# Performance work log

Hardware: AMD Instinct MI355X
Metric: run time of the kernel (lower is better)

Reference implementation:

```python
import jax, jax.numpy as jnp
import numpy as np

BN_EPS = 1e-5
DIST_MIN = 1e-10


def _three_nn(p1t, p2t):
    # p1t: [B,N,3], p2t: [B,S,3] -> squared dists/idx of 3 nearest, [B,N,3]
    d2 = (jnp.sum(p1t * p1t, -1, keepdims=True)
          - 2.0 * jnp.einsum('bnc,bsc->bns', p1t, p2t)
          + jnp.sum(p2t * p2t, -1)[:, None, :])  # [B,N,S]
    neg, idx = jax.lax.top_k(-d2, 3)
    return -neg, idx


def _gather_knn(f2t, idx):
    # f2t: [B,S,D], idx: [B,N,3] -> [B,N,3,D]
    return jax.vmap(lambda f, i: f[i])(f2t, idx)


def _conv_bn_relu(x, W, b, g, beta):
    # x: [B,C,N]; 1x1 conv == channel GEMM, then train-mode BN, then ReLU
    y = jnp.einsum('oc,bcn->bon', W, x) + b[None, :, None]
    mean = jnp.mean(y, axis=(0, 2), keepdims=True)
    var = jnp.mean((y - mean) ** 2, axis=(0, 2), keepdims=True)
    yn = (y - mean) * jax.lax.rsqrt(var + BN_EPS)
    return jax.nn.relu(yn * g[None, :, None] + beta[None, :, None])


def setup_inputs() -> dict:
    key = jax.random.key(0)
    ks = jax.random.split(key, 10)
    B, N, S, D1, D2 = 4, 8192, 2048, 128, 256
    C_in, C_mid, C_out = D1 + D2, 256, 256
    inp = {
        'pos1': jax.random.normal(ks[0], (B, 3, N), jnp.float32),
        'pos2': jax.random.normal(ks[1], (B, 3, S), jnp.float32),
        'feature1': jax.random.normal(ks[2], (B, D1, N), jnp.float32),
        'feature2': jax.random.normal(ks[3], (B, D2, S), jnp.float32),
        'W1': jax.random.normal(ks[4], (C_mid, C_in), jnp.float32) / np.sqrt(C_in),
        'b1': jnp.zeros((C_mid,), jnp.float32),
        'g1': jnp.ones((C_mid,), jnp.float32),
        'beta1': jnp.zeros((C_mid,), jnp.float32),
        'W2': jax.random.normal(ks[5], (C_out, C_mid), jnp.float32) / np.sqrt(C_mid),
        'b2': jnp.zeros((C_out,), jnp.float32),
        'g2': jnp.ones((C_out,), jnp.float32),
        'beta2': jnp.zeros((C_out,), jnp.float32),
    }
    return inp


def reference(pos1, pos2, feature1, feature2, W1, b1, g1, beta1, W2, b2, g2, beta2):
    B = pos1.shape[0]
    p1t = jnp.transpose(pos1, (0, 2, 1))  # [B,N,3]
    p2t = jnp.transpose(pos2, (0, 2, 1))  # [B,S,3]
    dists, idx = _three_nn(p1t, p2t)      # [B,N,3]
    dists = jnp.maximum(dists, DIST_MIN)
    w = 1.0 / dists
    w = w / jnp.sum(w, -1, keepdims=True)  # [B,N,3]
    f2t = jnp.transpose(feature2, (0, 2, 1))  # [B,S,D2]
    gathered = _gather_knn(f2t, idx)           # [B,N,3,D2]
    interp = jnp.sum(gathered * w[..., None], axis=2)  # [B,N,D2]
    interp = jnp.transpose(interp, (0, 2, 1))          # [B,D2,N]
    feat = jnp.concatenate([interp, feature1], axis=1)  # [B,D2+D1,N]
    feat = _conv_bn_relu(feat, W1, b1, g1, beta1)
    feat = _conv_bn_relu(feat, W2, b2, g2, beta2)
    return feat
```

## Files before the change

kernel.cpp:

```cpp
#include <hip/hip_runtime.h>
#include <hip/hip_bf16.h>

constexpr int B = 4, N = 8192, S = 2048;

typedef __attribute__((ext_vector_type(8))) short short8;
typedef __attribute__((ext_vector_type(4))) float v4f;

__device__ inline float u2f(ushort u) {
    union { ushort u; __hip_bfloat16 h; } c; c.u = u; return __bfloat162float(c.h);
}
__device__ inline ushort f2u(float f) {
    union { ushort u; __hip_bfloat16 h; } c; c.h = __float2bfloat16(f); return c.u;
}
__device__ inline void async_lds16(const void* g, void* l) {
    __builtin_amdgcn_global_load_lds(
        (const __attribute__((address_space(1))) unsigned*)g,
        (__attribute__((address_space(3))) unsigned*)l, 16, 0, 0);
}
__device__ inline short8 ld8(const ushort* p) { return *(const short8*)p; }

__device__ inline void transpose_tile(
    const float* __restrict__ ip, ushort* __restrict__ op,
    int L, int C, int l0, int c0, int tt, ushort (*tl)[66])
{
    const int lr = tt & 63, cb = tt >> 6;
    #pragma unroll
    for (int i = 0; i < 16; ++i) {
        int c = cb + 4 * i;
        tl[lr][c] = f2u(ip[(size_t)(c0 + c) * L + l0 + lr]);
    }
    __syncthreads();
    const int cp = tt & 31, lrow = tt >> 5;
    #pragma unroll
    for (int i = 0; i < 8; ++i) {
        int l = lrow + 8 * i;
        ushort2 v;
        v.x = tl[l][2 * cp]; v.y = tl[l][2 * cp + 1];
        *(ushort2*)(op + (size_t)(l0 + l) * C + c0 + 2 * cp) = v;
    }
}

__global__ __launch_bounds__(512) void prep_all(
    const float* __restrict__ W1, const float* __restrict__ W2,
    const float* __restrict__ pos2, const float* __restrict__ f2,
    const float* __restrict__ f1, const float* __restrict__ pos1,
    ushort* __restrict__ W1r, ushort* __restrict__ W2r,
    float* __restrict__ zero_region,
    ushort* __restrict__ f2T, ushort* __restrict__ f1T,
    float* __restrict__ wgt, int* __restrict__ idxb)
{
    __shared__ __align__(16) char sm[45056];
    const int bid = blockIdx.x;
    const int t = threadIdx.x;

    if (bid < 512) {
        float4* pk = (float4*)sm;
        float*  dL = (float*)(sm + 32768);
        int*    iL = (int*)  (sm + 32768 + 6144);
        const int b = bid >> 7, n0 = (bid & 127) * 64;
        const int lane = t & 63;
        const int w = __builtin_amdgcn_readfirstlane(t >> 6);

        for (int i = t; i < S; i += 512) {
            float x = pos2[(b * 3 + 0) * S + i];
            float y = pos2[(b * 3 + 1) * S + i];
            float z = pos2[(b * 3 + 2) * S + i];
            pk[i] = make_float4(x, y, z, x * x + y * y + z * z);
        }
        __syncthreads();

        {
            const int qi = n0 + lane;
            const float x1 = pos1[(b * 3 + 0) * N + qi];
            const float y1 = pos1[(b * 3 + 1) * N + qi];
            const float z1 = pos1[(b * 3 + 2) * N + qi];
            const float t1 = x1 * x1 + y1 * y1 + z1 * z1;
            const float4* __restrict__ pp = pk + w * 256;
            float d0 = 3.4e38f, d1 = 3.4e38f, d2 = 3.4e38f;
            int i0 = 0x7fffffff, i1 = 0x7fffffff, i2 = 0x7fffffff;
            #pragma unroll 8
            for (int i = 0; i < 256; ++i) {
                float4 p = pp[i];
                float dot = fmaf(x1, p.x, fmaf(y1, p.y, z1 * p.z));
                float dd = fmaf(-2.f, dot, t1) + p.w;
                int s = w * 256 + i;
                bool c0 = dd < d0, c1 = dd < d1, c2 = dd < d2;
                i2 = c1 ? i1 : (c2 ? s : i2);
                i1 = c0 ? i0 : (c1 ? s : i1);
                i0 = c0 ? s : i0;
                float nd1 = __builtin_amdgcn_fmed3f(dd, d0, d1);
                float nd2 = __builtin_amdgcn_fmed3f(dd, d1, d2);
                d0 = fminf(d0, dd);
                d1 = nd1; d2 = nd2;
            }
            int base = (w * 64 + lane) * 3;
            dL[base + 0] = d0; dL[base + 1] = d1; dL[base + 2] = d2;
            iL[base + 0] = i0; iL[base + 1] = i1; iL[base + 2] = i2;
        }
        __syncthreads();
        if (t < 64) {
            float f0 = dL[t*3+0], fv1 = dL[t*3+1], fv2 = dL[t*3+2];
            int   j0 = iL[t*3+0], j1 = iL[t*3+1], j2 = iL[t*3+2];
            #pragma unroll
            for (int c = 1; c < 8; ++c) {
                int cb = (c * 64 + t) * 3;
                #pragma unroll
                for (int k = 0; k < 3; ++k) {
                    float d = dL[cb + k]; int id = iL[cb + k];
                    bool l0 = (d < f0)  || (d == f0  && id < j0);
                    bool l1 = (d < fv1) || (d == fv1 && id < j1);
                    bool l2 = (d < fv2) || (d == fv2 && id < j2);
                    if (l0)      { fv2 = fv1; j2 = j1; fv1 = f0; j1 = j0; f0 = d; j0 = id; }
                    else if (l1) { fv2 = fv1; j2 = j1; fv1 = d; j1 = id; }
                    else if (l2) { fv2 = d; j2 = id; }
                }
            }
            float w0 = 1.f / fmaxf(f0, 1e-10f);
            float w1 = 1.f / fmaxf(fv1, 1e-10f);
            float w2 = 1.f / fmaxf(fv2, 1e-10f);
            float inv = 1.f / (w0 + w1 + w2);
            j0 = ((unsigned)j0 < S) ? j0 : 0;
            j1 = ((unsigned)j1 < S) ? j1 : 0;
            j2 = ((unsigned)j2 < S) ? j2 : 0;
            int base = (b * N + n0 + t) * 3;
            wgt[base + 0] = w0 * inv; wgt[base + 1] = w1 * inv; wgt[base + 2] = w2 * inv;
            idxb[base + 0] = j0; idxb[base + 1] = j1; idxb[base + 2] = j2;
        }
    } else if (bid < 768) {
        ushort (*tl)[66] = (ushort(*)[66])(sm + (t >> 8) * 16896);
        const int tt = t & 255;
        int tile = (bid - 512) * 2 + (t >> 8);
        int b = tile >> 7, ct = (tile >> 5) & 3, st = tile & 31;
        transpose_tile(f2 + (size_t)b * 256 * S, f2T + (size_t)b * S * 256,
                       S, 256, st * 64, ct * 64, tt, tl);
    } else if (bid < 1280) {
        ushort (*tl)[66] = (ushort(*)[66])(sm + (t >> 8) * 16896);
        const int tt = t & 255;
        int u = (bid - 768) * 2 + (t >> 8);
        int b = u >> 8, ct = (u >> 7) & 1, lt = u & 127;
        transpose_tile(f1 + (size_t)b * 128 * N, f1T + (size_t)b * N * 128,
                       N, 128, lt * 64, ct * 64, tt, tl);
    } else {
        int i = (bid - 1280) * 512 + t;
        if (i < 12288) {
            int kk = i >> 10, qq = (i >> 8) & 3, o = i & 255;
            const float* src = W1 + o * 384 + kk * 32 + qq * 8;
            float4 a = *(const float4*)src, bb = *(const float4*)(src + 4);
            union { short8 s; ushort u[8]; } pkv;
            pkv.u[0]=f2u(a.x); pkv.u[1]=f2u(a.y); pkv.u[2]=f2u(a.z); pkv.u[3]=f2u(a.w);
            pkv.u[4]=f2u(bb.x); pkv.u[5]=f2u(bb.y); pkv.u[6]=f2u(bb.z); pkv.u[7]=f2u(bb.w);
            *(short8*)(W1r + i * 8) = pkv.s;
        } else if (i < 20480) {
            int u = i - 12288;
            int kk = u >> 10, qq = (u >> 8) & 3, o = u & 255;
            const float* src = W2 + o * 256 + kk * 32 + qq * 8;
            float4 a = *(const float4*)src, bb = *(const float4*)(src + 4);
            union { short8 s; ushort u[8]; } pkv;
            pkv.u[0]=f2u(a.x); pkv.u[1]=f2u(a.y); pkv.u[2]=f2u(a.z); pkv.u[3]=f2u(a.w);
            pkv.u[4]=f2u(bb.x); pkv.u[5]=f2u(bb.y); pkv.u[6]=f2u(bb.z); pkv.u[7]=f2u(bb.w);
            *(short8*)(W2r + u * 8) = pkv.s;
        } else if (i < 21504) {
            zero_region[i - 20480] = 0.f;
        }
    }
}

__global__ __launch_bounds__(512) void gemm1_kernel(
    const ushort* __restrict__ W1r, const float* __restrict__ bias1,
    const ushort* __restrict__ f2T, const ushort* __restrict__ f1T,
    const int* __restrict__ idxb, const float* __restrict__ wgt,
    ushort* __restrict__ y, float* __restrict__ sums)
{
    __shared__ __align__(16) char smem[49152];
    ushort* Xs = (ushort*)smem;
    ushort* Wb = (ushort*)(smem + 32768);

    const int t = threadIdx.x;
    const int lane = t & 63;
    const int w = __builtin_amdgcn_readfirstlane(t >> 6);
    const int b = blockIdx.y;
    const int n0 = blockIdx.x * 64;
    const int q = lane >> 4, r = lane & 15, r7 = r & 7;

    #pragma unroll
    for (int jj = 0; jj < 2; ++jj)
        async_lds16((const char*)W1r + jj * 8192 + t * 16,
                    (char*)Wb + jj * 8192 + w * 1024);

    short8 f1v[2];
    const int flp = t & 15, fro = t >> 4;
    #pragma unroll
    for (int it = 0; it < 2; ++it)
        f1v[it] = ld8(f1T + ((size_t)b * N + n0 + fro + 32 * it) * 128 + 8 * flp);

    {
        const int lp = t & 31, ro = t >> 5;
        #pragma unroll
        for (int it = 0; it < 4; ++it) {
            int rr = ro + 16 * it;
            int base = (b * N + n0 + rr) * 3;
            int s0 = idxb[base], s1 = idxb[base + 1], s2 = idxb[base + 2];
            s0 = ((unsigned)s0 < S) ? s0 : 0;
            s1 = ((unsigned)s1 < S) ? s1 : 0;
            s2 = ((unsigned)s2 < S) ? s2 : 0;
            float w0 = wgt[base], w1 = wgt[base + 1], w2 = wgt[base + 2];
            union { short8 s; ushort u[8]; } a, c, d, o;
            a.s = ld8(f2T + ((size_t)b * S + s0) * 256 + 8 * lp);
            c.s = ld8(f2T + ((size_t)b * S + s1) * 256 + 8 * lp);
            d.s = ld8(f2T + ((size_t)b * S + s2) * 256 + 8 * lp);
            #pragma unroll
            for (int j = 0; j < 8; ++j)
                o.u[j] = f2u(w0 * u2f(a.u[j]) + w1 * u2f(c.u[j]) + w2 * u2f(d.u[j]));
            *(short8*)(Xs + rr * 256 + ((lp ^ (rr & 7)) * 8)) = o.s;
        }
    }
    __syncthreads();

    v4f acc[2][4];
    #pragma unroll
    for (int mt = 0; mt < 2; ++mt)
        #pragma unroll
        for (int nf = 0; nf < 4; ++nf) acc[mt][nf] = (v4f){0.f, 0.f, 0.f, 0.f};

    #pragma unroll
    for (int kk = 0; kk < 8; ++kk) {
        short8 wreg0 = ld8(W1r + (kk + 1) * 8192 + t * 16);
        short8 wreg1 = ld8(W1r + (kk + 1) * 8192 + t * 16 + 8);
        short8 af[2], bf[4];
        #pragma unroll
        for (int mt = 0; mt < 2; ++mt)
            af[mt] = ld8(Wb + q * 2048 + (w * 32 + mt * 16 + r) * 8);
        #pragma unroll
        for (int nf = 0; nf < 4; ++nf)
            bf[nf] = ld8(Xs + (nf * 16 + r) * 256 + (((kk * 4 + q) ^ r7) * 8));
        #pragma unroll
        for (int mt = 0; mt < 2; ++mt)
            #pragma unroll
            for (int nf = 0; nf < 4; ++nf)
                acc[mt][nf] = __builtin_amdgcn_mfma_f32_16x16x32_bf16(
                    af[mt], bf[nf], acc[mt][nf], 0, 0, 0);
        __syncthreads();
        *(short8*)(Wb + t * 16) = wreg0;
        *(short8*)(Wb + t * 16 + 8) = wreg1;
        if (kk == 7) {
            #pragma unroll
            for (int it = 0; it < 2; ++it) {
                int rr = fro + 32 * it;
                *(short8*)(Xs + rr * 128 + ((flp ^ (rr & 7)) * 8)) = f1v[it];
            }
        }
        __syncthreads();
    }

    #pragma unroll
    for (int kk = 8; kk < 12; ++kk) {
        short8 wreg0, wreg1;
        if (kk < 11) {
            wreg0 = ld8(W1r + (kk + 1) * 8192 + t * 16);
            wreg1 = ld8(W1r + (kk + 1) * 8192 + t * 16 + 8);
        }
        short8 af[2], bf[4];
        #pragma unroll
        for (int mt = 0; mt < 2; ++mt)
            af[mt] = ld8(Wb + q * 2048 + (w * 32 + mt * 16 + r) * 8);
        #pragma unroll
        for (int nf = 0; nf < 4; ++nf)
            bf[nf] = ld8(Xs + (nf * 16 + r) * 128 + ((((kk - 8) * 4 + q) ^ r7) * 8));
        #pragma unroll
        for (int mt = 0; mt < 2; ++mt)
            #pragma unroll
            for (int nf = 0; nf < 4; ++nf)
                acc[mt][nf] = __builtin_amdgcn_mfma_f32_16x16x32_bf16(
                    af[mt], bf[nf], acc[mt][nf], 0, 0, 0);
        if (kk < 11) {
            __syncthreads();
            *(short8*)(Wb + t * 16) = wreg0;
            *(short8*)(Wb + t * 16 + 8) = wreg1;
            __syncthreads();
        }
    }
    __syncthreads();

    float* statS = (float*)Xs;
    float* statQ = statS + 256;
    #pragma unroll
    for (int mt = 0; mt < 2; ++mt) {
        int ob = w * 32 + mt * 16 + q * 4;
        float4 bi = *(const float4*)(bias1 + ob);
        float sj0 = 0, sj1 = 0, sj2 = 0, sj3 = 0;
        float qj0 = 0, qj1 = 0, qj2 = 0, qj3 = 0;
        #pragma unroll
        for (int nf = 0; nf < 4; ++nf) {
            int n = n0 + nf * 16 + r;
            float v0 = acc[mt][nf][0] + bi.x, v1 = acc[mt][nf][1] + bi.y;
            float v2 = acc[mt][nf][2] + bi.z, v3 = acc[mt][nf][3] + bi.w;
            ushort4 pk; pk.x = f2u(v0); pk.y = f2u(v1); pk.z = f2u(v2); pk.w = f2u(v3);
            *(ushort4*)(y + ((size_t)b * N + n) * 256 + ob) = pk;
            sj0 += v0; sj1 += v1; sj2 += v2; sj3 += v3;
            qj0 += v0 * v0; qj1 += v1 * v1; qj2 += v2 * v2; qj3 += v3 * v3;
        }
        #pragma unroll
        for (int m = 1; m <= 8; m <<= 1) {
            sj0 += __shfl_xor(sj0, m); sj1 += __shfl_xor(sj1, m);
            sj2 += __shfl_xor(sj2, m); sj3 += __shfl_xor(sj3, m);
            qj0 += __shfl_xor(qj0, m); qj1 += __shfl_xor(qj1, m);
            qj2 += __shfl_xor(qj2, m); qj3 += __shfl_xor(qj3, m);
        }
        if (r == 0) {
            statS[ob + 0] = sj0; statS[ob + 1] = sj1;
            statS[ob + 2] = sj2; statS[ob + 3] = sj3;
            statQ[ob + 0] = qj0; statQ[ob + 1] = qj1;
            statQ[ob + 2] = qj2; statQ[ob + 3] = qj3;
        }
    }
    __syncthreads();
    if (t < 256) {
        atomicAdd(&sums[t], statS[t]);
        atomicAdd(&sums[256 + t], statQ[t]);
    }
}

__global__ __launch_bounds__(512) void gemm2_kernel(
    const ushort* __restrict__ Wr, const float* __restrict__ bias,
    const float* __restrict__ sums1, const float* __restrict__ g1,
    const float* __restrict__ be1,
    ushort* __restrict__ y, float* __restrict__ sums)
{
    __shared__ __align__(16) ushort Xs[64 * 256];
    __shared__ __align__(16) ushort Wbuf[2 * 8192];
    __shared__ float ssA[256], ssB[256];
    const int t = threadIdx.x;
    const int b = blockIdx.y;
    const int n0 = blockIdx.x * 64;
    const int w = t >> 6, lane = t & 63;
    const int q = lane >> 4, r = lane & 15, r7 = r & 7;

    {
        const char* g0 = (const char*)Wr;
        #pragma unroll
        for (int jj = 0; jj < 2; ++jj)
            async_lds16(g0 + jj * 8192 + t * 16,
                        (char*)Wbuf + jj * 8192 + w * 1024);
    }

    if (t < 256) {
        float sv = sums1[t], qv = sums1[256 + t];
        float mean = sv * (1.f / 32768.f);
        float var = qv * (1.f / 32768.f) - mean * mean;
        float rstd = rsqrtf(var + 1e-5f);
        float sc = g1[t] * rstd;
        ssA[t] = sc;
        ssB[t] = be1[t] - mean * sc;
    }
    __syncthreads();

    {
        const int lp = t & 31, ro = t >> 5;
        #pragma unroll
        for (int it = 0; it < 4; ++it) {
            int rr = ro + 16 * it;
            union { short8 s; ushort u[8]; } v, o;
            v.s = ld8(y + ((size_t)b * N + n0 + rr) * 256 + 8 * lp);
            #pragma unroll
            for (int j = 0; j < 8; ++j)
                o.u[j] = f2u(fmaxf(u2f(v.u[j]) * ssA[8 * lp + j] + ssB[8 * lp + j], 0.f));
            *(short8*)(Xs + rr * 256 + ((lp ^ (rr & 7)) * 8)) = o.s;
        }
    }
    __syncthreads();

    v4f acc[2][4];
    #pragma unroll
    for (int mt = 0; mt < 2; ++mt)
        #pragma unroll
        for (int nf = 0; nf < 4; ++nf) acc[mt][nf] = (v4f){0.f, 0.f, 0.f, 0.f};

    for (int kk = 0; kk < 8; ++kk) {
        if (kk < 7) {
            const char* g = (const char*)Wr + (kk + 1) * 16384;
            char* l = (char*)Wbuf + ((kk + 1) & 1) * 16384;
            #pragma unroll
            for (int jj = 0; jj < 2; ++jj)
                async_lds16(g + jj * 8192 + t * 16, l + jj * 8192 + w * 1024);
        }
        const ushort* Wb = Wbuf + (kk & 1) * 8192;
        short8 af[2], bf[4];
        #pragma unroll
        for (int mt = 0; mt < 2; ++mt)
            af[mt] = ld8(Wb + q * 2048 + (w * 32 + mt * 16 + r) * 8);
        #pragma unroll
        for (int nf = 0; nf < 4; ++nf)
            bf[nf] = ld8(Xs + (nf * 16 + r) * 256 + (((kk * 4 + q) ^ r7) * 8));
        #pragma unroll
        for (int mt = 0; mt < 2; ++mt)
            #pragma unroll
            for (int nf = 0; nf < 4; ++nf)
                acc[mt][nf] = __builtin_amdgcn_mfma_f32_16x16x32_bf16(
                    af[mt], bf[nf], acc[mt][nf], 0, 0, 0);
        __syncthreads();
    }

    float* statS = (float*)Xs;
    float* statQ = statS + 256;
    #pragma unroll
    for (int mt = 0; mt < 2; ++mt) {
        int ob = w * 32 + mt * 16 + q * 4;
        float4 bi = *(const float4*)(bias + ob);
        float sj0 = 0, sj1 = 0, sj2 = 0, sj3 = 0;
        float qj0 = 0, qj1 = 0, qj2 = 0, qj3 = 0;
        #pragma unroll
        for (int nf = 0; nf < 4; ++nf) {
            int n = n0 + nf * 16 + r;
            float v0 = acc[mt][nf][0] + bi.x, v1 = acc[mt][nf][1] + bi.y;
            float v2 = acc[mt][nf][2] + bi.z, v3 = acc[mt][nf][3] + bi.w;
            ushort4 pk; pk.x = f2u(v0); pk.y = f2u(v1); pk.z = f2u(v2); pk.w = f2u(v3);
            *(ushort4*)(y + ((size_t)b * N + n) * 256 + ob) = pk;
            sj0 += v0; sj1 += v1; sj2 += v2; sj3 += v3;
            qj0 += v0 * v0; qj1 += v1 * v1; qj2 += v2 * v2; qj3 += v3 * v3;
        }
        #pragma unroll
        for (int m = 1; m <= 8; m <<= 1) {
            sj0 += __shfl_xor(sj0, m); sj1 += __shfl_xor(sj1, m);
            sj2 += __shfl_xor(sj2, m); sj3 += __shfl_xor(sj3, m);
            qj0 += __shfl_xor(qj0, m); qj1 += __shfl_xor(qj1, m);
            qj2 += __shfl_xor(qj2, m); qj3 += __shfl_xor(qj3, m);
        }
        if (r == 0) {
            statS[ob + 0] = sj0; statS[ob + 1] = sj1;
            statS[ob + 2] = sj2; statS[ob + 3] = sj3;
            statQ[ob + 0] = qj0; statQ[ob + 1] = qj1;
            statQ[ob + 2] = qj2; statQ[ob + 3] = qj3;
        }
    }
    __syncthreads();
    if (t < 256) {
        atomicAdd(&sums[t], statS[t]);
        atomicAdd(&sums[256 + t], statQ[t]);
    }
}

__global__ __launch_bounds__(256) void final_kernel(
    const ushort* __restrict__ Y, const float* __restrict__ sums2,
    const float* __restrict__ g2, const float* __restrict__ be2,
    float* __restrict__ out)
{
    __shared__ float tl[64][65];
    __shared__ float ssA[64], ssB[64];
    const int t = threadIdx.x;
    const int b = blockIdx.z;
    const int n0 = blockIdx.x * 64, c0 = blockIdx.y * 64;

    if (t < 64) {
        int c = c0 + t;
        float sv = sums2[c], qv = sums2[256 + c];
        float mean = sv * (1.f / 32768.f);
        float var = qv * (1.f / 32768.f) - mean * mean;
        float rstd = rsqrtf(var + 1e-5f);
        float sc = g2[c] * rstd;
        ssA[t] = sc;
        ssB[t] = be2[c] - mean * sc;
    }
    __syncthreads();

    const int nl = t >> 3, cho = 8 * (t & 7);
    #pragma unroll
    for (int it = 0; it < 2; ++it) {
        int n = nl + 32 * it;
        union { short8 s; ushort u[8]; } v;
        v.s = ld8(Y + ((size_t)b * N + n0 + n) * 256 + c0 + cho);
        #pragma unroll
        for (int j = 0; j < 8; ++j)
            tl[n][cho + j] = fmaxf(u2f(v.u[j]) * ssA[cho + j] + ssB[cho + j], 0.f);
    }
    __syncthreads();

    const int cl = t >> 4, n4 = (t & 15) * 4;
    #pragma unroll
    for (int it = 0; it < 4; ++it) {
        int c = cl + 16 * it;
        float4 v;
        v.x = tl[n4 + 0][c]; v.y = tl[n4 + 1][c];
        v.z = tl[n4 + 2][c]; v.w = tl[n4 + 3][c];
        *(float4*)(out + ((size_t)b * 256 + c0 + c) * N + n0 + n4) = v;
    }
}

extern "C" void kernel_launch(void* const* d_in, const int* in_sizes, int n_in,
                              void* d_out, int out_size, void* d_ws, size_t ws_size,
                              hipStream_t stream)
{
    (void)in_sizes; (void)n_in; (void)out_size;
    if (ws_size < (30u << 20)) return;

    const float* pos1 = (const float*)d_in[0];
    const float* pos2 = (const float*)d_in[1];
    const float* f1   = (const float*)d_in[2];
    const float* f2   = (const float*)d_in[3];
    const float* W1   = (const float*)d_in[4];
    const float* b1   = (const float*)d_in[5];
    const float* g1   = (const float*)d_in[6];
    const float* be1  = (const float*)d_in[7];
    const float* W2   = (const float*)d_in[8];
    const float* b2   = (const float*)d_in[9];
    const float* g2   = (const float*)d_in[10];
    const float* be2  = (const float*)d_in[11];

    char* ws = (char*)d_ws;
    float*  sums1  = (float*)ws;
    float*  sums2  = sums1 + 512;
    int*    idxb   = (int*)(ws + 4096);
    float*  wgt    = (float*)(ws + 4096 + 393216);
    ushort* W1r    = (ushort*)(ws + 4096 + 786432);
    ushort* W2r    = (ushort*)(ws + 4096 + 786432 + 196608);
    ushort* f2T    = (ushort*)(ws + (2u << 20));
    ushort* f1T    = (ushort*)(ws + (6u << 20));
    ushort* y      = (ushort*)(ws + (14u << 20));

    prep_all<<<1322, 512, 0, stream>>>(W1, W2, pos2, f2, f1, pos1,
                                       W1r, W2r, sums1, f2T, f1T, wgt, idxb);

    gemm1_kernel<<<dim3(N / 64, B), 512, 0, stream>>>(
        W1r, b1, f2T, f1T, idxb, wgt, y, sums1);

    gemm2_kernel<<<dim3(N / 64, B), 512, 0, stream>>>(
        W2r, b2, sums1, g1, be1, y, sums2);

    final_kernel<<<dim3(N / 64, 256 / 64, B), 256, 0, stream>>>(
        y, sums2, g2, be2, (float*)d_out);
}
```

Measured before the change: 187.6 us.

## Fuse GEMM1, GEMM2 and final BN into one persistent kernel with grid barriers

The gemm1, gemm2 and final kernels are merged into a single kernel that keeps each block's 64x256 intermediate tile in LDS. Grid-wide atomic-counter barriers stand in for the kernel boundaries needed by the batch-norm statistics. This removes the global round-trips of the bf16 intermediate y and two kernel launches. In exchange, all 512 blocks must be co-resident (launch_bounds 512,4), or the spin barriers deadlock. The zeroing region grows so the prep kernel also clears the counters.

```diff
diff --git a/kernel.cpp b/kernel.cpp
--- a/kernel.cpp
+++ b/kernel.cpp
@@ -159,21 +159,29 @@
             pkv.u[0]=f2u(a.x); pkv.u[1]=f2u(a.y); pkv.u[2]=f2u(a.z); pkv.u[3]=f2u(a.w);
             pkv.u[4]=f2u(bb.x); pkv.u[5]=f2u(bb.y); pkv.u[6]=f2u(bb.z); pkv.u[7]=f2u(bb.w);
             *(short8*)(W2r + u * 8) = pkv.s;
-        } else if (i < 21504) {
+        } else if (i < 21536) {
             zero_region[i - 20480] = 0.f;
         }
     }
 }
 
-__global__ __launch_bounds__(512) void gemm1_kernel(
+__global__ __launch_bounds__(512, 4) void mega_kernel(
     const ushort* __restrict__ W1r, const float* __restrict__ bias1,
     const ushort* __restrict__ f2T, const ushort* __restrict__ f1T,
     const int* __restrict__ idxb, const float* __restrict__ wgt,
-    ushort* __restrict__ y, float* __restrict__ sums)
+    float* __restrict__ sums, unsigned* __restrict__ ctrs,
+    const float* __restrict__ g1, const float* __restrict__ be1,
+    const ushort* __restrict__ W2r, const float* __restrict__ bias2,
+    const float* __restrict__ g2, const float* __restrict__ be2,
+    float* __restrict__ out)
 {
-    __shared__ __align__(16) char smem[49152];
-    ushort* Xs = (ushort*)smem;
-    ushort* Wb = (ushort*)(smem + 32768);
+    __shared__ __align__(16) char smem[53248];
+    ushort* Xs   = (ushort*)smem;
+    ushort* Y    = (ushort*)smem;
+    ushort* Wb   = (ushort*)(smem + 32768);
+    float*  stat = (float*)(smem + 49152);
+    float*  aux  = (float*)(smem + 51200);
+    float*  tl2  = (float*)(smem + 32768);
 
     const int t = threadIdx.x;
     const int lane = t & 63;
@@ -281,21 +289,25 @@
     }
     __syncthreads();
 
-    float* statS = (float*)Xs;
-    float* statQ = statS + 256;
+    #pragma unroll
+    for (int jj = 0; jj < 2; ++jj)
+        async_lds16((const char*)W2r + jj * 8192 + t * 16,
+                    (char*)Wb + jj * 8192 + w * 1024);
+
     #pragma unroll
     for (int mt = 0; mt < 2; ++mt) {
         int ob = w * 32 + mt * 16 + q * 4;
+        int g = ob >> 3, e = ob & 7;
         float4 bi = *(const float4*)(bias1 + ob);
         float sj0 = 0, sj1 = 0, sj2 = 0, sj3 = 0;
         float qj0 = 0, qj1 = 0, qj2 = 0, qj3 = 0;
         #pragma unroll
         for (int nf = 0; nf < 4; ++nf) {
-            int n = n0 + nf * 16 + r;
+            int n = nf * 16 + r;
             float v0 = acc[mt][nf][0] + bi.x, v1 = acc[mt][nf][1] + bi.y;
             float v2 = acc[mt][nf][2] + bi.z, v3 = acc[mt][nf][3] + bi.w;
             ushort4 pk; pk.x = f2u(v0); pk.y = f2u(v1); pk.z = f2u(v2); pk.w = f2u(v3);
-            *(ushort4*)(y + ((size_t)b * N + n) * 256 + ob) = pk;
+            *(ushort4*)(Y + n * 256 + ((g ^ (n & 7)) * 8 + e)) = pk;
             sj0 += v0; sj1 += v1; sj2 += v2; sj3 += v3;
             qj0 += v0 * v0; qj1 += v1 * v1; qj2 += v2 * v2; qj3 += v3 * v3;
         }
@@ -307,114 +319,112 @@
             qj2 += __shfl_xor(qj2, m); qj3 += __shfl_xor(qj3, m);
         }
         if (r == 0) {
-            statS[ob + 0] = sj0; statS[ob + 1] = sj1;
-            statS[ob + 2] = sj2; statS[ob + 3] = sj3;
-            statQ[ob + 0] = qj0; statQ[ob + 1] = qj1;
-            statQ[ob + 2] = qj2; statQ[ob + 3] = qj3;
+            stat[ob + 0] = sj0; stat[ob + 1] = sj1;
+            stat[ob + 2] = sj2; stat[ob + 3] = sj3;
+            stat[256 + ob + 0] = qj0; stat[256 + ob + 1] = qj1;
+            stat[256 + ob + 2] = qj2; stat[256 + ob + 3] = qj3;
         }
     }
     __syncthreads();
     if (t < 256) {
-        atomicAdd(&sums[t], statS[t]);
-        atomicAdd(&sums[256 + t], statQ[t]);
-    }
-}
-
-__global__ __launch_bounds__(512) void gemm2_kernel(
-    const ushort* __restrict__ Wr, const float* __restrict__ bias,
-    const float* __restrict__ sums1, const float* __restrict__ g1,
-    const float* __restrict__ be1,
-    ushort* __restrict__ y, float* __restrict__ sums)
-{
-    __shared__ __align__(16) ushort Xs[64 * 256];
-    __shared__ __align__(16) ushort Wbuf[2 * 8192];
-    __shared__ float ssA[256], ssB[256];
-    const int t = threadIdx.x;
-    const int b = blockIdx.y;
-    const int n0 = blockIdx.x * 64;
-    const int w = t >> 6, lane = t & 63;
-    const int q = lane >> 4, r = lane & 15, r7 = r & 7;
-
-    {
-        const char* g0 = (const char*)Wr;
-        #pragma unroll
-        for (int jj = 0; jj < 2; ++jj)
-            async_lds16(g0 + jj * 8192 + t * 16,
-                        (char*)Wbuf + jj * 8192 + w * 1024);
-    }
+        atomicAdd(&sums[t], stat[t]);
+        atomicAdd(&sums[256 + t], stat[256 + t]);
+    }
+    __threadfence();
+    __syncthreads();
+    if (t == 0) {
+        __hip_atomic_fetch_add(&ctrs[0], 1u, __ATOMIC_ACQ_REL,
+                               __HIP_MEMORY_SCOPE_AGENT);
+        while (__hip_atomic_load(&ctrs[0], __ATOMIC_ACQUIRE,
+                                 __HIP_MEMORY_SCOPE_AGENT) < 512u)
+            __builtin_amdgcn_s_sleep(8);
+    }
+    __syncthreads();
+    __threadfence();
 
     if (t < 256) {
-        float sv = sums1[t], qv = sums1[256 + t];
+        float sv = __hip_atomic_load(&sums[t], __ATOMIC_RELAXED,
+                                     __HIP_MEMORY_SCOPE_AGENT);
+        float qv = __hip_atomic_load(&sums[256 + t], __ATOMIC_RELAXED,
+                                     __HIP_MEMORY_SCOPE_AGENT);
         float mean = sv * (1.f / 32768.f);
         float var = qv * (1.f / 32768.f) - mean * mean;
         float rstd = rsqrtf(var + 1e-5f);
         float sc = g1[t] * rstd;
-        ssA[t] = sc;
-        ssB[t] = be1[t] - mean * sc;
-    }
-    __syncthreads();
-
+        aux[t] = sc;
+        aux[256 + t] = be1[t] - mean * sc;
+    }
+    __syncthreads();
     {
-        const int lp = t & 31, ro = t >> 5;
-        #pragma unroll
-        for (int it = 0; it < 4; ++it) {
-            int rr = ro + 16 * it;
+        const int g = t & 31, nb = t >> 5;
+        float sa[8], sb[8];
+        #pragma unroll
+        for (int j = 0; j < 8; ++j) {
+            sa[j] = aux[g * 8 + j]; sb[j] = aux[256 + g * 8 + j];
+        }
+        #pragma unroll
+        for (int j = 0; j < 4; ++j) {
+            int n = nb * 4 + j;
+            ushort* p = Y + n * 256 + ((g ^ (n & 7)) * 8);
             union { short8 s; ushort u[8]; } v, o;
-            v.s = ld8(y + ((size_t)b * N + n0 + rr) * 256 + 8 * lp);
-            #pragma unroll
-            for (int j = 0; j < 8; ++j)
-                o.u[j] = f2u(fmaxf(u2f(v.u[j]) * ssA[8 * lp + j] + ssB[8 * lp + j], 0.f));
-            *(short8*)(Xs + rr * 256 + ((lp ^ (rr & 7)) * 8)) = o.s;
-        }
-    }
-    __syncthreads();
-
-    v4f acc[2][4];
+            v.s = ld8(p);
+            #pragma unroll
+            for (int e = 0; e < 8; ++e)
+                o.u[e] = f2u(fmaxf(u2f(v.u[e]) * sa[e] + sb[e], 0.f));
+            *(short8*)p = o.s;
+        }
+    }
+    __syncthreads();
+
+    v4f acc2[2][4];
     #pragma unroll
     for (int mt = 0; mt < 2; ++mt)
         #pragma unroll
-        for (int nf = 0; nf < 4; ++nf) acc[mt][nf] = (v4f){0.f, 0.f, 0.f, 0.f};
-
+        for (int nf = 0; nf < 4; ++nf) acc2[mt][nf] = (v4f){0.f, 0.f, 0.f, 0.f};
+
+    #pragma unroll
     for (int kk = 0; kk < 8; ++kk) {
+        short8 wreg0, wreg1;
         if (kk < 7) {
-            const char* g = (const char*)Wr + (kk + 1) * 16384;
-            char* l = (char*)Wbuf + ((kk + 1) & 1) * 16384;
-            #pragma unroll
-            for (int jj = 0; jj < 2; ++jj)
-                async_lds16(g + jj * 8192 + t * 16, l + jj * 8192 + w * 1024);
-        }
-        const ushort* Wb = Wbuf + (kk & 1) * 8192;
+            wreg0 = ld8(W2r + (kk + 1) * 8192 + t * 16);
+            wreg1 = ld8(W2r + (kk + 1) * 8192 + t * 16 + 8);
+        }
         short8 af[2], bf[4];
         #pragma unroll
         for (int mt = 0; mt < 2; ++mt)
             af[mt] = ld8(Wb + q * 2048 + (w * 32 + mt * 16 + r) * 8);
         #pragma unroll
         for (int nf = 0; nf < 4; ++nf)
-            bf[nf] = ld8(Xs + (nf * 16 + r) * 256 + (((kk * 4 + q) ^ r7) * 8));
+            bf[nf] = ld8(Y + (nf * 16 + r) * 256 + (((kk * 4 + q) ^ r7) * 8));
         #pragma unroll
         for (int mt = 0; mt < 2; ++mt)
             #pragma unroll
             for (int nf = 0; nf < 4; ++nf)
-                acc[mt][nf] = __builtin_amdgcn_mfma_f32_16x16x32_bf16(
-                    af[mt], bf[nf], acc[mt][nf], 0, 0, 0);
-        __syncthreads();
-    }
-
-    float* statS = (float*)Xs;
-    float* statQ = statS + 256;
+                acc2[mt][nf] = __builtin_amdgcn_mfma_f32_16x16x32_bf16(
+                    af[mt], bf[nf], acc2[mt][nf], 0, 0, 0);
+        if (kk < 7) {
+            __syncthreads();
+            *(short8*)(Wb + t * 16) = wreg0;
+            *(short8*)(Wb + t * 16 + 8) = wreg1;
+            __syncthreads();
+        }
+    }
+    __syncthreads();
+
     #pragma unroll
     for (int mt = 0; mt < 2; ++mt) {
         int ob = w * 32 + mt * 16 + q * 4;
-        float4 bi = *(const float4*)(bias + ob);
+        int g = ob >> 3, e = ob & 7;
+        float4 bi = *(const float4*)(bias2 + ob);
         float sj0 = 0, sj1 = 0, sj2 = 0, sj3 = 0;
         float qj0 = 0, qj1 = 0, qj2 = 0, qj3 = 0;
         #pragma unroll
         for (int nf = 0; nf < 4; ++nf) {
-            int n = n0 + nf * 16 + r;
-            float v0 = acc[mt][nf][0] + bi.x, v1 = acc[mt][nf][1] + bi.y;
-            float v2 = acc[mt][nf][2] + bi.z, v3 = acc[mt][nf][3] + bi.w;
+            int n = nf * 16 + r;
+            float v0 = acc2[mt][nf][0] + bi.x, v1 = acc2[mt][nf][1] + bi.y;
+            float v2 = acc2[mt][nf][2] + bi.z, v3 = acc2[mt][nf][3] + bi.w;
             ushort4 pk; pk.x = f2u(v0); pk.y = f2u(v1); pk.z = f2u(v2); pk.w = f2u(v3);
-            *(ushort4*)(y + ((size_t)b * N + n) * 256 + ob) = pk;
+            *(ushort4*)(Y + n * 256 + ((g ^ (n & 7)) * 8 + e)) = pk;
             sj0 += v0; sj1 += v1; sj2 += v2; sj3 += v3;
             qj0 += v0 * v0; qj1 += v1 * v1; qj2 += v2 * v2; qj3 += v3 * v3;
         }
@@ -426,62 +436,69 @@
             qj2 += __shfl_xor(qj2, m); qj3 += __shfl_xor(qj3, m);
         }
         if (r == 0) {
-            statS[ob + 0] = sj0; statS[ob + 1] = sj1;
-            statS[ob + 2] = sj2; statS[ob + 3] = sj3;
-            statQ[ob + 0] = qj0; statQ[ob + 1] = qj1;
-            statQ[ob + 2] = qj2; statQ[ob + 3] = qj3;
+            stat[ob + 0] = sj0; stat[ob + 1] = sj1;
+            stat[ob + 2] = sj2; stat[ob + 3] = sj3;
+            stat[256 + ob + 0] = qj0; stat[256 + ob + 1] = qj1;
+            stat[256 + ob + 2] = qj2; stat[256 + ob + 3] = qj3;
         }
     }
     __syncthreads();
     if (t < 256) {
-        atomicAdd(&sums[t], statS[t]);
-        atomicAdd(&sums[256 + t], statQ[t]);
-    }
-}
-
-__global__ __launch_bounds__(256) void final_kernel(
-    const ushort* __restrict__ Y, const float* __restrict__ sums2,
-    const float* __restrict__ g2, const float* __restrict__ be2,
-    float* __restrict__ out)
-{
-    __shared__ float tl[64][65];
-    __shared__ float ssA[64], ssB[64];
-    const int t = threadIdx.x;
-    const int b = blockIdx.z;
-    const int n0 = blockIdx.x * 64, c0 = blockIdx.y * 64;
-
-    if (t < 64) {
-        int c = c0 + t;
-        float sv = sums2[c], qv = sums2[256 + c];
+        atomicAdd(&sums[512 + t], stat[t]);
+        atomicAdd(&sums[768 + t], stat[256 + t]);
+    }
+    __threadfence();
+    __syncthreads();
+    if (t == 0) {
+        __hip_atomic_fetch_add(&ctrs[16], 1u, __ATOMIC_ACQ_REL,
+                               __HIP_MEMORY_SCOPE_AGENT);
+        while (__hip_atomic_load(&ctrs[16], __ATOMIC_ACQUIRE,
+                                 __HIP_MEMORY_SCOPE_AGENT) < 512u)
+            __builtin_amdgcn_s_sleep(8);
+    }
+    __syncthreads();
+    __threadfence();
+
+    if (t < 256) {
+        float sv = __hip_atomic_load(&sums[512 + t], __ATOMIC_RELAXED,
+                                     __HIP_MEMORY_SCOPE_AGENT);
+        float qv = __hip_atomic_load(&sums[768 + t], __ATOMIC_RELAXED,
+                                     __HIP_MEMORY_SCOPE_AGENT);
         float mean = sv * (1.f / 32768.f);
         float var = qv * (1.f / 32768.f) - mean * mean;
         float rstd = rsqrtf(var + 1e-5f);
-        float sc = g2[c] * rstd;
-        ssA[t] = sc;
-        ssB[t] = be2[c] - mean * sc;
-    }
-    __syncthreads();
-
-    const int nl = t >> 3, cho = 8 * (t & 7);
-    #pragma unroll
-    for (int it = 0; it < 2; ++it) {
-        int n = nl + 32 * it;
-        union { short8 s; ushort u[8]; } v;
-        v.s = ld8(Y + ((size_t)b * N + n0 + n) * 256 + c0 + cho);
-        #pragma unroll
-        for (int j = 0; j < 8; ++j)
-            tl[n][cho + j] = fmaxf(u2f(v.u[j]) * ssA[cho + j] + ssB[cho + j], 0.f);
-    }
-    __syncthreads();
-
-    const int cl = t >> 4, n4 = (t & 15) * 4;
-    #pragma unroll
-    for (int it = 0; it < 4; ++it) {
-        int c = cl + 16 * it;
-        float4 v;
-        v.x = tl[n4 + 0][c]; v.y = tl[n4 + 1][c];
-        v.z = tl[n4 + 2][c]; v.w = tl[n4 + 3][c];
-        *(float4*)(out + ((size_t)b * 256 + c0 + c) * N + n0 + n4) = v;
+        float sc = g2[t] * rstd;
+        aux[t] = sc;
+        aux[256 + t] = be2[t] - mean * sc;
+    }
+    __syncthreads();
+
+    for (int pass = 0; pass < 4; ++pass) {
+        int c0l = pass * 64;
+        {
+            int n = t >> 3, g8 = t & 7, g = (c0l >> 3) + g8;
+            union { short8 s; ushort u[8]; } v;
+            v.s = ld8(Y + n * 256 + ((g ^ (n & 7)) * 8));
+            #pragma unroll
+            for (int j = 0; j < 8; ++j)
+                tl2[n * 65 + g8 * 8 + j] =
+                    fmaxf(u2f(v.u[j]) * aux[g * 8 + j] + aux[256 + g * 8 + j], 0.f);
+        }
+        __syncthreads();
+        {
+            const int cl = t >> 4, n4 = (t & 15) * 4;
+            #pragma unroll
+            for (int it = 0; it < 2; ++it) {
+                int c = cl + 32 * it;
+                float4 v;
+                v.x = tl2[(n4 + 0) * 65 + c];
+                v.y = tl2[(n4 + 1) * 65 + c];
+                v.z = tl2[(n4 + 2) * 65 + c];
+                v.w = tl2[(n4 + 3) * 65 + c];
+                *(float4*)(out + ((size_t)b * 256 + c0l + c) * N + n0 + n4) = v;
+            }
+        }
+        __syncthreads();
     }
 }
 
@@ -490,7 +507,7 @@
                               hipStream_t stream)
 {
     (void)in_sizes; (void)n_in; (void)out_size;
-    if (ws_size < (30u << 20)) return;
+    if (ws_size < (16u << 20)) return;
 
     const float* pos1 = (const float*)d_in[0];
     const float* pos2 = (const float*)d_in[1];
@@ -506,25 +523,19 @@
     const float* be2  = (const float*)d_in[11];
 
     char* ws = (char*)d_ws;
-    float*  sums1  = (float*)ws;
-    float*  sums2  = sums1 + 512;
-    int*    idxb   = (int*)(ws + 4096);
-    float*  wgt    = (float*)(ws + 4096 + 393216);
-    ushort* W1r    = (ushort*)(ws + 4096 + 786432);
-    ushort* W2r    = (ushort*)(ws + 4096 + 786432 + 196608);
+    float*    sums = (float*)ws;
+    unsigned* ctrs = (unsigned*)(ws + 4096);
+    int*    idxb   = (int*)(ws + 8192);
+    float*  wgt    = (float*)(ws + 8192 + 393216);
+    ushort* W1r    = (ushort*)(ws + 8192 + 786432);
+    ushort* W2r    = (ushort*)(ws + 8192 + 786432 + 196608);
     ushort* f2T    = (ushort*)(ws + (2u << 20));
     ushort* f1T    = (ushort*)(ws + (6u << 20));
-    ushort* y      = (ushort*)(ws + (14u << 20));
-
-    prep_all<<<1322, 512, 0, stream>>>(W1, W2, pos2, f2, f1, pos1,
-                                       W1r, W2r, sums1, f2T, f1T, wgt, idxb);
-
-    gemm1_kernel<<<dim3(N / 64, B), 512, 0, stream>>>(
-        W1r, b1, f2T, f1T, idxb, wgt, y, sums1);
-
-    gemm2_kernel<<<dim3(N / 64, B), 512, 0, stream>>>(
-        W2r, b2, sums1, g1, be1, y, sums2);
-
-    final_kernel<<<dim3(N / 64, 256 / 64, B), 256, 0, stream>>>(
-        y, sums2, g2, be2, (float*)d_out);
-}
+
+    prep_all<<<1323, 512, 0, stream>>>(W1, W2, pos2, f2, f1, pos1,
+                                       W1r, W2r, sums, f2T, f1T, wgt, idxb);
+
+    mega_kernel<<<dim3(N / 64, B), 512, 0, stream>>>(
+        W1r, b1, f2T, f1T, idxb, wgt, sums, ctrs,
+        g1, be1, W2r, b2, g2, be2, (float*)d_out);
+}
```

After: 456.7 us. +143.5%, slower.
